# Optimization experiments

Hardware: AMD Instinct MI355X
Metric: run time of the kernel (lower is better)

## Reference

```python
import jax, jax.numpy as jnp
import numpy as np

DIM = 2048
CTX_DIM = 4096
NUM_HEADS = 16
HEAD_DIM = DIM // NUM_HEADS
EPS = 1e-6


def _rms_norm(x, weight, eps=EPS):
    # RMSNorm over last dim with learned weight (native dtype path for fp32)
    var = jnp.mean(jnp.square(x), axis=-1, keepdims=True)
    return x * jax.lax.rsqrt(var + eps) * weight


def setup_inputs() -> dict:
    key = jax.random.key(0)
    ks = jax.random.split(key, 12)
    B, L, S = 1, 8192, 512
    sd_q = 1.0 / np.sqrt(DIM)
    sd_c = 1.0 / np.sqrt(CTX_DIM)
    return {
        "x": jax.random.normal(ks[0], (B, L, DIM), dtype=jnp.float32),
        "context": jax.random.normal(ks[1], (B, S, CTX_DIM), dtype=jnp.float32),
        "Wq": jax.random.normal(ks[2], (DIM, DIM), dtype=jnp.float32) * sd_q,
        "bq": jax.random.normal(ks[3], (DIM,), dtype=jnp.float32) * 0.01,
        "Wk": jax.random.normal(ks[4], (CTX_DIM, DIM), dtype=jnp.float32) * sd_c,
        "bk": jax.random.normal(ks[5], (DIM,), dtype=jnp.float32) * 0.01,
        "Wv": jax.random.normal(ks[6], (CTX_DIM, DIM), dtype=jnp.float32) * sd_c,
        "bv": jax.random.normal(ks[7], (DIM,), dtype=jnp.float32) * 0.01,
        "Wo": jax.random.normal(ks[8], (DIM, DIM), dtype=jnp.float32) * sd_q,
        "bo": jax.random.normal(ks[9], (DIM,), dtype=jnp.float32) * 0.01,
        "g_q": jnp.ones((DIM,), dtype=jnp.float32),
        "g_k": jnp.ones((DIM,), dtype=jnp.float32),
    }


def reference(x, context, Wq, bq, Wk, bk, Wv, bv, Wo, bo, g_q, g_k):
    B, L, C = x.shape
    S = context.shape[1]
    # QKV projections + RMSNorm on Q,K (over full model dim, pre head split)
    q = _rms_norm(x @ Wq + bq, g_q)           # [B, L, C]
    k = _rms_norm(context @ Wk + bk, g_k)     # [B, S, C]
    v = context @ Wv + bv                     # [B, S, C]
    # split heads
    q = q.reshape(B, L, NUM_HEADS, HEAD_DIM)
    k = k.reshape(B, S, NUM_HEADS, HEAD_DIM)
    v = v.reshape(B, S, NUM_HEADS, HEAD_DIM)
    # non-causal SDPA
    scale = 1.0 / np.sqrt(HEAD_DIM)
    scores = jnp.einsum("blhd,bshd->bhls", q, k) * scale
    probs = jax.nn.softmax(scores, axis=-1)
    attn = jnp.einsum("bhls,bshd->blhd", probs, v).reshape(B, L, C)
    return attn @ Wo + bo
```

## Files before the change

kernel.cpp:

```cpp
#include <hip/hip_runtime.h>
#include <hip/hip_bf16.h>
#include <stdint.h>

#define L_SEQ 8192
#define S_SEQ 512
#define DIM   2048
#define CTX   4096
#define NH    16
#define HD    128

typedef __bf16 bf16_t;
typedef bf16_t bf16x8 __attribute__((ext_vector_type(8)));
typedef float  f32x4_t __attribute__((ext_vector_type(4)));
typedef float  f32x16_t __attribute__((ext_vector_type(16)));

__device__ __forceinline__ ushort f2b(float f) {
  union { float f; uint32_t u; } v; v.f = f;
  uint32_t u = v.u;
  uint32_t r = (u + 0x7fffu + ((u >> 16) & 1u)) >> 16;
  return (ushort)r;
}
__device__ __forceinline__ uint32_t pk2(float a, float b) {
  return (uint32_t)f2b(a) | ((uint32_t)f2b(b) << 16);
}
__device__ __forceinline__ float b2f(ushort u) {
  union { uint32_t u; float f; } v; v.u = ((uint32_t)u) << 16;
  return v.f;
}
__device__ __forceinline__ void gll16(const ushort* g, ushort* l) {
  __builtin_amdgcn_global_load_lds((const __attribute__((address_space(1))) void*)g,
                                   (__attribute__((address_space(3))) void*)l, 16, 0, 0);
}

__global__ __launch_bounds__(256) void k_cast(const float* __restrict__ in,
                                              ushort* __restrict__ out) {
  const size_t i = ((size_t)blockIdx.x * 256 + threadIdx.x) * 8;
  float4 a = *(const float4*)(in + i);
  float4 b = *(const float4*)(in + i + 4);
  uint4 r;
  r.x = pk2(a.x, a.y); r.y = pk2(a.z, a.w);
  r.z = pk2(b.x, b.y); r.w = pk2(b.z, b.w);
  *(uint4*)(out + i) = r;
}

__global__ __launch_bounds__(256) void k_tcast(const float* __restrict__ src,
                                               ushort* __restrict__ dst, int K, int N) {
  __shared__ float t[32][33];
  int tx = threadIdx.x, ty = threadIdx.y;
  int n0 = blockIdx.x * 32, k0 = blockIdx.y * 32;
#pragma unroll
  for (int i = 0; i < 4; i++)
    t[ty + 8 * i][tx] = src[(size_t)(k0 + ty + 8 * i) * N + n0 + tx];
  __syncthreads();
#pragma unroll
  for (int i = 0; i < 4; i++)
    dst[(size_t)(n0 + ty + 8 * i) * K + k0 + tx] = f2b(t[tx][ty + 8 * i]);
}

__global__ __launch_bounds__(256) void k_rmsnorm(const ushort* __restrict__ in,
                                                 ushort* __restrict__ out,
                                                 const float* __restrict__ g, float scale) {
  const int row = blockIdx.x, tid = threadIdx.x;
  uint4 v = *(const uint4*)(in + (size_t)row * DIM + tid * 8);
  const uint32_t* vu = (const uint32_t*)&v;
  float f[8];
#pragma unroll
  for (int i = 0; i < 4; i++) {
    f[2 * i]     = b2f((ushort)(vu[i] & 0xffffu));
    f[2 * i + 1] = b2f((ushort)(vu[i] >> 16));
  }
  float s = 0.f;
#pragma unroll
  for (int i = 0; i < 8; i++) s += f[i] * f[i];
#pragma unroll
  for (int off = 32; off; off >>= 1) s += __shfl_down(s, off);
  __shared__ float wsum[4];
  __shared__ float rtot;
  if ((tid & 63) == 0) wsum[tid >> 6] = s;
  __syncthreads();
  if (tid == 0)
    rtot = rsqrtf((wsum[0] + wsum[1] + wsum[2] + wsum[3]) * (1.0f / DIM) + 1e-6f);
  __syncthreads();
  const float rms = rtot * scale;
  const float* gp = g + tid * 8;
  float4 g0 = *(const float4*)gp, g1 = *(const float4*)(gp + 4);
  ushort r[8];
  r[0] = f2b(f[0] * rms * g0.x); r[1] = f2b(f[1] * rms * g0.y);
  r[2] = f2b(f[2] * rms * g0.z); r[3] = f2b(f[3] * rms * g0.w);
  r[4] = f2b(f[4] * rms * g1.x); r[5] = f2b(f[5] * rms * g1.y);
  r[6] = f2b(f[6] * rms * g1.z); r[7] = f2b(f[7] * rms * g1.w);
  *(uint4*)(out + (size_t)row * DIM + tid * 8) = *(uint4*)r;
}

template <int OUT_MODE>
__global__ __launch_bounds__(512, 2) void k_gemm256(const ushort* __restrict__ A,
                                                    const ushort* __restrict__ Bt,
                                                    const float* __restrict__ bias,
                                                    void* __restrict__ outp,
                                                    int M, int N, int K) {
  __shared__ __align__(16) ushort lds[65536];
  const int tid = threadIdx.x;
  const int l = tid & 63, wid = tid >> 6;
  const int wm = wid >> 2, wn = wid & 3;
  const int lr = l & 15, lq = l >> 4;

  const int nwg = gridDim.x * gridDim.y;
  const int bid = blockIdx.y * gridDim.x + blockIdx.x;
  const int swz = (bid & 7) * (nwg >> 3) + (bid >> 3);
  const int m0 = (swz / gridDim.x) * 256, n0 = (swz % gridDim.x) * 256;

  f32x4_t acc[8][4];
#pragma unroll
  for (int i = 0; i < 8; i++)
#pragma unroll
    for (int j = 0; j < 4; j++) acc[i][j] = f32x4_t{0.f, 0.f, 0.f, 0.f};

  const int srow = l >> 3;
  const int schunk = ((l & 7) ^ (srow & 7)) * 8;
  auto stage = [&](int buf, int tile, int mat, int h) {
    const ushort* gp = mat ? Bt : A;
    const int rn0 = mat ? n0 : m0;
    const size_t r0 = (size_t)(rn0 + h * 128 + wid * 8 + srow);
    const ushort* g0 = gp + r0 * K + tile * 64 + schunk;
    ushort* l0 = &lds[buf * 32768 + mat * 16384 + (h * 128 + wid * 8) * 64];
    gll16(g0, l0);
    gll16(g0 + (size_t)64 * K, l0 + 64 * 64);
  };

  auto rdA = [&](int buf, int mf, int ks) -> bf16x8 {
    const int R = wm * 128 + mf * 16 + lr;
    return *(const bf16x8*)(&lds[buf * 32768 + R * 64 + (((ks * 4 + lq) ^ (R & 7)) * 8)]);
  };
  auto rdB = [&](int buf, int nf, int ks) -> bf16x8 {
    const int R = wn * 64 + nf * 16 + lr;
    return *(const bf16x8*)(&lds[buf * 32768 + 16384 + R * 64 + (((ks * 4 + lq) ^ (R & 7)) * 8)]);
  };

  const int NT = K >> 6;
  stage(0, 0, 0, 0); stage(0, 0, 0, 1); stage(0, 0, 1, 0); stage(0, 0, 1, 1);

  bf16x8 a[4][2], a2[4][2], b[2][2], b2[2][2];
  for (int kt = 0; kt < NT; kt++) {
    const int cur = kt & 1, nxt = cur ^ 1;
    const bool pf = (kt + 1 < NT);
    if (pf) { stage(nxt, kt + 1, 0, 0); asm volatile("s_waitcnt vmcnt(2)" ::: "memory"); }
    else    { asm volatile("s_waitcnt vmcnt(0)" ::: "memory"); }
    __builtin_amdgcn_sched_barrier(0);
    __builtin_amdgcn_s_barrier();
    __builtin_amdgcn_sched_barrier(0);
#pragma unroll
    for (int mf = 0; mf < 4; mf++) { a[mf][0] = rdA(cur, mf, 0); a[mf][1] = rdA(cur, mf, 1); }
#pragma unroll
    for (int nf = 0; nf < 2; nf++) { b[nf][0] = rdB(cur, nf, 0); b[nf][1] = rdB(cur, nf, 1); }
    __builtin_amdgcn_s_setprio(1);
#pragma unroll
    for (int mf = 0; mf < 4; mf++)
#pragma unroll
      for (int nf = 0; nf < 2; nf++) {
        acc[mf][nf] = __builtin_amdgcn_mfma_f32_16x16x32_bf16(a[mf][0], b[nf][0], acc[mf][nf], 0, 0, 0);
        acc[mf][nf] = __builtin_amdgcn_mfma_f32_16x16x32_bf16(a[mf][1], b[nf][1], acc[mf][nf], 0, 0, 0);
      }
    __builtin_amdgcn_s_setprio(0);
    __builtin_amdgcn_sched_barrier(0);
    __builtin_amdgcn_s_barrier();
    __builtin_amdgcn_sched_barrier(0);
#pragma unroll
    for (int mf = 0; mf < 4; mf++) { a2[mf][0] = rdA(cur, mf + 4, 0); a2[mf][1] = rdA(cur, mf + 4, 1); }
    if (pf) stage(nxt, kt + 1, 0, 1);
    __builtin_amdgcn_sched_barrier(0);
    __builtin_amdgcn_s_barrier();
    __builtin_amdgcn_sched_barrier(0);
    __builtin_amdgcn_s_setprio(1);
#pragma unroll
    for (int mf = 0; mf < 4; mf++)
#pragma unroll
      for (int nf = 0; nf < 2; nf++) {
        acc[mf + 4][nf] = __builtin_amdgcn_mfma_f32_16x16x32_bf16(a2[mf][0], b[nf][0], acc[mf + 4][nf], 0, 0, 0);
        acc[mf + 4][nf] = __builtin_amdgcn_mfma_f32_16x16x32_bf16(a2[mf][1], b[nf][1], acc[mf + 4][nf], 0, 0, 0);
      }
    __builtin_amdgcn_s_setprio(0);
    __builtin_amdgcn_sched_barrier(0);
    __builtin_amdgcn_s_barrier();
    __builtin_amdgcn_sched_barrier(0);
#pragma unroll
    for (int nf = 0; nf < 2; nf++) { b2[nf][0] = rdB(cur, nf + 2, 0); b2[nf][1] = rdB(cur, nf + 2, 1); }
    if (pf) stage(nxt, kt + 1, 1, 0);
    __builtin_amdgcn_sched_barrier(0);
    __builtin_amdgcn_s_barrier();
    __builtin_amdgcn_sched_barrier(0);
    __builtin_amdgcn_s_setprio(1);
#pragma unroll
    for (int mf = 0; mf < 4; mf++)
#pragma unroll
      for (int nf = 0; nf < 2; nf++) {
        acc[mf + 4][nf + 2] = __builtin_amdgcn_mfma_f32_16x16x32_bf16(a2[mf][0], b2[nf][0], acc[mf + 4][nf + 2], 0, 0, 0);
        acc[mf + 4][nf + 2] = __builtin_amdgcn_mfma_f32_16x16x32_bf16(a2[mf][1], b2[nf][1], acc[mf + 4][nf + 2], 0, 0, 0);
      }
    __builtin_amdgcn_s_setprio(0);
    __builtin_amdgcn_sched_barrier(0);
    __builtin_amdgcn_s_barrier();
    __builtin_amdgcn_sched_barrier(0);
#pragma unroll
    for (int mf = 0; mf < 4; mf++) { a[mf][0] = rdA(cur, mf, 0); a[mf][1] = rdA(cur, mf, 1); }
    if (pf) stage(nxt, kt + 1, 1, 1);
    __builtin_amdgcn_sched_barrier(0);
    __builtin_amdgcn_s_barrier();
    __builtin_amdgcn_sched_barrier(0);
    __builtin_amdgcn_s_setprio(1);
#pragma unroll
    for (int mf = 0; mf < 4; mf++)
#pragma unroll
      for (int nf = 0; nf < 2; nf++) {
        acc[mf][nf + 2] = __builtin_amdgcn_mfma_f32_16x16x32_bf16(a[mf][0], b2[nf][0], acc[mf][nf + 2], 0, 0, 0);
        acc[mf][nf + 2] = __builtin_amdgcn_mfma_f32_16x16x32_bf16(a[mf][1], b2[nf][1], acc[mf][nf + 2], 0, 0, 0);
      }
    __builtin_amdgcn_s_setprio(0);
    __builtin_amdgcn_sched_barrier(0);
    __builtin_amdgcn_s_barrier();
    __builtin_amdgcn_sched_barrier(0);
  }

#pragma unroll
  for (int nf = 0; nf < 4; nf++) {
    const int col = n0 + wn * 64 + nf * 16 + lr;
    const float bv = bias[col];
#pragma unroll
    for (int mf = 0; mf < 8; mf++) {
#pragma unroll
      for (int r = 0; r < 4; r++) {
        const int row = m0 + wm * 128 + mf * 16 + lq * 4 + r;
        const float v = acc[mf][nf][r] + bv;
        if constexpr (OUT_MODE == 0)
          ((float*)outp)[(size_t)row * N + col] = v;
        else
          ((ushort*)outp)[(size_t)row * N + col] = f2b(v);
      }
    }
  }
}

template <int OUT_MODE>
__global__ __launch_bounds__(256) void k_gemm_bt(const ushort* __restrict__ A,
                                                 const ushort* __restrict__ Bt,
                                                 const float* __restrict__ bias,
                                                 const float* __restrict__ bias2,
                                                 void* __restrict__ outp,
                                                 void* __restrict__ outp2,
                                                 int M, int N, int K) {
  __shared__ __align__(16) ushort As[128 * 32];
  __shared__ __align__(16) ushort Bs[128 * 32];
  const int tid = threadIdx.x;
  const int l = tid & 63, wid = tid >> 6;
  const int wr = wid >> 1, wc = wid & 1;
  const int lr = l & 15, lq = l >> 4;

  const int nwg = gridDim.x * gridDim.y;
  const int bid = blockIdx.y * gridDim.x + blockIdx.x;
  const int swz = (bid & 7) * (nwg >> 3) + (bid >> 3);
  const int m0 = (swz / gridDim.x) * 128, n0 = (swz % gridDim.x) * 128;

  f32x4_t acc[4][4];
#pragma unroll
  for (int i = 0; i < 4; i++)
#pragma unroll
    for (int j = 0; j < 4; j++) acc[i][j] = f32x4_t{0.f, 0.f, 0.f, 0.f};

  const int srow = l >> 2;
  const int scol = (l & 3) * 8;
  const ushort* ga0 = A  + (size_t)(m0 + wid * 16 + srow) * K + scol;
  const ushort* ga1 = A  + (size_t)(m0 + (4 + wid) * 16 + srow) * K + scol;
  const ushort* gb0 = Bt + (size_t)(n0 + wid * 16 + srow) * K + scol;
  const ushort* gb1 = Bt + (size_t)(n0 + (4 + wid) * 16 + srow) * K + scol;
  ushort* la0 = &As[wid * 512];
  ushort* la1 = &As[(4 + wid) * 512];
  ushort* lb0 = &Bs[wid * 512];
  ushort* lb1 = &Bs[(4 + wid) * 512];

  const int NT = K >> 5;
  for (int kt = 0; kt < NT; kt++) {
    __syncthreads();
    const int ko = kt * 32;
    gll16(ga0 + ko, la0);
    gll16(ga1 + ko, la1);
    gll16(gb0 + ko, lb0);
    gll16(gb1 + ko, lb1);
    __syncthreads();

    bf16x8 af[4], bfr[4];
#pragma unroll
    for (int mi = 0; mi < 4; mi++)
      af[mi] = *(const bf16x8*)(&As[(wr * 64 + mi * 16 + lr) * 32 + lq * 8]);
#pragma unroll
    for (int ni = 0; ni < 4; ni++)
      bfr[ni] = *(const bf16x8*)(&Bs[(wc * 64 + ni * 16 + lr) * 32 + lq * 8]);
#pragma unroll
    for (int mi = 0; mi < 4; mi++)
#pragma unroll
      for (int ni = 0; ni < 4; ni++)
        acc[mi][ni] = __builtin_amdgcn_mfma_f32_16x16x32_bf16(af[mi], bfr[ni], acc[mi][ni], 0, 0, 0);
  }

#pragma unroll
  for (int mi = 0; mi < 4; mi++) {
#pragma unroll
    for (int ni = 0; ni < 4; ni++) {
      const int col = n0 + wc * 64 + ni * 16 + lr;
      float bv;
      if constexpr (OUT_MODE == 3) bv = (col < DIM) ? bias[col] : bias2[col - DIM];
      else bv = bias[col];
#pragma unroll
      for (int r = 0; r < 4; r++) {
        const int row = m0 + wr * 64 + mi * 16 + lq * 4 + r;
        const float v = acc[mi][ni][r] + bv;
        if constexpr (OUT_MODE == 0)
          ((float*)outp)[(size_t)row * N + col] = v;
        else if constexpr (OUT_MODE == 1)
          ((ushort*)outp)[(size_t)row * N + col] = f2b(v);
        else {
          if (col < DIM) ((ushort*)outp)[(size_t)row * DIM + col] = f2b(v);
          else ((ushort*)outp2)[(size_t)(col - DIM) * M + row] = f2b(v);
        }
      }
    }
  }
}

__global__ __launch_bounds__(256) void k_attn(const ushort* __restrict__ Qb,
                                              const ushort* __restrict__ Kb,
                                              const ushort* __restrict__ Vt,
                                              ushort* __restrict__ Ob) {
  __shared__ __align__(16) ushort smem[16384];
  ushort* Ks = smem;
  ushort* Vs = smem + 64 * 128;

  const int tid = threadIdx.x;
  const int l = tid & 63, wid = tid >> 6;
  const int lo = l & 31, hi = l >> 5;

  const int bid = blockIdx.x;
  const int swz = (bid & 7) * 128 + (bid >> 3);
  const int h = swz >> 6;
  const int q0 = (swz & 63) * 128 + wid * 32;

  bf16x8 qf[8];
  {
    const ushort* qp = Qb + (size_t)(q0 + lo) * DIM + h * HD + hi * 8;
#pragma unroll
    for (int ds = 0; ds < 8; ds++) qf[ds] = *(const bf16x8*)(qp + ds * 16);
  }

  f32x16_t o[4] = {};
  float m_run = -1e30f, l_run = 0.f;

  for (int kvb = 0; kvb < S_SEQ / 64; kvb++) {
    __syncthreads();
#pragma unroll
    for (int i = 0; i < 4; i++) {
      const int c = i * 256 + tid, row = c >> 4, cs = c & 15;
      gll16(Kb + (size_t)(kvb * 64 + row) * DIM + h * HD + ((cs ^ (row & 7)) * 8),
            Ks + c * 8);
    }
#pragma unroll
    for (int i = 0; i < 4; i++) {
      const int c = i * 256 + tid, row = c >> 3, cs = c & 7;
      gll16(Vt + (size_t)(h * HD + row) * S_SEQ + kvb * 64 + ((cs ^ (row & 7)) * 8),
            Vs + c * 8);
    }
    __syncthreads();

    f32x16_t sA = {}, sB = {};
#pragma unroll
    for (int ds = 0; ds < 8; ds++) {
      const int ch = ((hi + ds * 2) ^ (lo & 7)) * 8;
      bf16x8 kA = *(const bf16x8*)(Ks + lo * 128 + ch);
      bf16x8 kB = *(const bf16x8*)(Ks + (32 + lo) * 128 + ch);
      sA = __builtin_amdgcn_mfma_f32_32x32x16_bf16(kA, qf[ds], sA, 0, 0, 0);
      sB = __builtin_amdgcn_mfma_f32_32x32x16_bf16(kB, qf[ds], sB, 0, 0, 0);
    }

    float p[32];
#pragma unroll
    for (int i = 0; i < 16; i++) { p[i] = sA[i]; p[16 + i] = sB[i]; }
    float pm = p[0];
#pragma unroll
    for (int i = 1; i < 32; i++) pm = fmaxf(pm, p[i]);
    pm = fmaxf(pm, __shfl_xor(pm, 32));
    const float mn = fmaxf(m_run, pm);
    const float corr = __expf(m_run - mn);
    m_run = mn;
    float ps = 0.f;
#pragma unroll
    for (int i = 0; i < 32; i++) { p[i] = __expf(p[i] - mn); ps += p[i]; }
    ps += __shfl_xor(ps, 32);
    l_run = l_run * corr + ps;
#pragma unroll
    for (int nt = 0; nt < 4; nt++) o[nt] *= corr;

    uint32_t c[16];
#pragma unroll
    for (int j = 0; j < 16; j++) c[j] = pk2(p[2 * j], p[2 * j + 1]);
    bf16x8 pf[4];
#pragma unroll
    for (int s = 0; s < 4; s++) {
      const uint32_t ca = c[4 * s], cb = c[4 * s + 1], cc = c[4 * s + 2], cd = c[4 * s + 3];
      const uint32_t sa = __shfl_xor(ca, 32), sb = __shfl_xor(cb, 32);
      const uint32_t sc = __shfl_xor(cc, 32), sd = __shfl_xor(cd, 32);
      union { uint32_t u[4]; bf16x8 v; } f;
      f.u[0] = hi ? sc : ca; f.u[1] = hi ? sd : cb;
      f.u[2] = hi ? cc : sa; f.u[3] = hi ? cd : sb;
      pf[s] = f.v;
    }

#pragma unroll
    for (int nt = 0; nt < 4; nt++) {
      const int vrow = nt * 32 + lo;
#pragma unroll
      for (int s = 0; s < 4; s++) {
        bf16x8 vf = *(const bf16x8*)(Vs + vrow * 64 + (((s * 2 + hi) ^ (lo & 7)) * 8));
        o[nt] = __builtin_amdgcn_mfma_f32_32x32x16_bf16(vf, pf[s], o[nt], 0, 0, 0);
      }
    }
  }

  const float inv = 1.0f / l_run;
#pragma unroll
  for (int nt = 0; nt < 4; nt++) o[nt] *= inv;

  __syncthreads();
  float* tb = (float*)smem + wid * (32 * 33);
  const int q2 = l >> 1, dh = (l & 1) * 16;
#pragma unroll
  for (int nt = 0; nt < 4; nt++) {
#pragma unroll
    for (int r = 0; r < 16; r++)
      tb[lo * 33 + ((r & 3) + 8 * (r >> 2) + 4 * hi)] = o[nt][r];
    asm volatile("s_waitcnt lgkmcnt(0)" ::: "memory");
    __builtin_amdgcn_sched_barrier(0);
    ushort tmp[16];
#pragma unroll
    for (int j = 0; j < 16; j++) tmp[j] = f2b(tb[q2 * 33 + dh + j]);
    asm volatile("s_waitcnt lgkmcnt(0)" ::: "memory");
    __builtin_amdgcn_sched_barrier(0);
    const size_t oaddr = (size_t)(q0 + q2) * DIM + h * HD + nt * 32 + dh;
    *(uint4*)(Ob + oaddr) = *(uint4*)tmp;
    *(uint4*)(Ob + oaddr + 8) = *(uint4*)(tmp + 8);
  }
}

extern "C" void kernel_launch(void* const* d_in, const int* in_sizes, int n_in,
                              void* d_out, int out_size, void* d_ws, size_t ws_size,
                              hipStream_t stream) {
  const float* x   = (const float*)d_in[0];
  const float* ctx = (const float*)d_in[1];
  const float* Wq  = (const float*)d_in[2];
  const float* bq  = (const float*)d_in[3];
  const float* Wk  = (const float*)d_in[4];
  const float* bk  = (const float*)d_in[5];
  const float* Wv  = (const float*)d_in[6];
  const float* bv  = (const float*)d_in[7];
  const float* Wo  = (const float*)d_in[8];
  const float* bo  = (const float*)d_in[9];
  const float* gq  = (const float*)d_in[10];
  const float* gk  = (const float*)d_in[11];

  char* ws = (char*)d_ws;
  ushort* wqt   = (ushort*)(ws);
  ushort* wkt   = (ushort*)(ws + 8388608);
  ushort* wvt   = (ushort*)(ws + 25165824);
  ushort* wot   = (ushort*)(ws + 41943040);
  ushort* qb    = (ushort*)(ws + 50331648);
  ushort* kb    = (ushort*)(ws + 83886080);
  ushort* vt    = (ushort*)(ws + 85983232);
  ushort* xb    = (ushort*)(ws + 88080384);
  ushort* ctxb  = (ushort*)(ws + 88080384);
  ushort* qraw  = (ushort*)(ws + 121634816);
  ushort* kraw  = (ushort*)(ws + 121634816);
  ushort* attnb = (ushort*)(ws + 121634816);

  k_cast<<<L_SEQ * DIM / 8 / 256, 256, 0, stream>>>(x, xb);
  k_tcast<<<dim3(DIM / 32, DIM / 32), dim3(32, 8), 0, stream>>>(Wq, wqt, DIM, DIM);
  k_tcast<<<dim3(DIM / 32, CTX / 32), dim3(32, 8), 0, stream>>>(Wk, wkt, CTX, DIM);
  k_tcast<<<dim3(DIM / 32, CTX / 32), dim3(32, 8), 0, stream>>>(Wv, wvt, CTX, DIM);
  k_tcast<<<dim3(DIM / 32, DIM / 32), dim3(32, 8), 0, stream>>>(Wo, wot, DIM, DIM);

  k_gemm256<1><<<dim3(DIM / 256, L_SEQ / 256), 512, 0, stream>>>(xb, wqt, bq, qraw, L_SEQ, DIM, DIM);
  k_cast<<<S_SEQ * CTX / 8 / 256, 256, 0, stream>>>(ctx, ctxb);
  k_rmsnorm<<<L_SEQ, 256, 0, stream>>>(qraw, qb, gq, 0.08838834764831843f);
  k_gemm_bt<3><<<dim3(2 * DIM / 128, S_SEQ / 128), 256, 0, stream>>>(ctxb, wkt, bk, bv, kraw, vt, S_SEQ, 2 * DIM, CTX);
  k_rmsnorm<<<S_SEQ, 256, 0, stream>>>(kraw, kb, gk, 1.0f);
  k_attn<<<L_SEQ / 128 * NH, 256, 0, stream>>>(qb, kb, vt, attnb);
  k_gemm256<0><<<dim3(DIM / 256, L_SEQ / 256), 512, 0, stream>>>(attnb, wot, bo, d_out, L_SEQ, DIM, DIM);
}
```

Measured before the change: 363.8 us.

## Double-buffer LDS tiles in bt GEMM to overlap global loads with MFMA

Doubles the LDS A/B tile buffers in the transposed-B GEMM kernel and prefetches the next k-tile via direct global-to-LDS loads while the current tile is consumed. Explicit vmcnt waits and scheduling barriers replace the previous load-then-sync pattern, aiming to hide global memory latency behind MFMA work. This doubles LDS use per block, which may reduce occupancy, and it depends on the vmcnt(4) count matching the four outstanding loads.

```diff
diff --git a/kernel.cpp b/kernel.cpp
--- a/kernel.cpp
+++ b/kernel.cpp
@@ -247,8 +247,8 @@
                                                  void* __restrict__ outp,
                                                  void* __restrict__ outp2,
                                                  int M, int N, int K) {
-  __shared__ __align__(16) ushort As[128 * 32];
-  __shared__ __align__(16) ushort Bs[128 * 32];
+  __shared__ __align__(16) ushort As[2 * 128 * 32];
+  __shared__ __align__(16) ushort Bs[2 * 128 * 32];
   const int tid = threadIdx.x;
   const int l = tid & 63, wid = tid >> 6;
   const int wr = wid >> 1, wc = wid & 1;
@@ -271,33 +271,41 @@
   const ushort* ga1 = A  + (size_t)(m0 + (4 + wid) * 16 + srow) * K + scol;
   const ushort* gb0 = Bt + (size_t)(n0 + wid * 16 + srow) * K + scol;
   const ushort* gb1 = Bt + (size_t)(n0 + (4 + wid) * 16 + srow) * K + scol;
-  ushort* la0 = &As[wid * 512];
-  ushort* la1 = &As[(4 + wid) * 512];
-  ushort* lb0 = &Bs[wid * 512];
-  ushort* lb1 = &Bs[(4 + wid) * 512];
+
+  auto stageAB = [&](int buf, int kt) {
+    const int ko = kt * 32;
+    gll16(ga0 + ko, &As[buf * 4096 + wid * 512]);
+    gll16(ga1 + ko, &As[buf * 4096 + (4 + wid) * 512]);
+    gll16(gb0 + ko, &Bs[buf * 4096 + wid * 512]);
+    gll16(gb1 + ko, &Bs[buf * 4096 + (4 + wid) * 512]);
+  };
 
   const int NT = K >> 5;
+  stageAB(0, 0);
   for (int kt = 0; kt < NT; kt++) {
-    __syncthreads();
-    const int ko = kt * 32;
-    gll16(ga0 + ko, la0);
-    gll16(ga1 + ko, la1);
-    gll16(gb0 + ko, lb0);
-    gll16(gb1 + ko, lb1);
-    __syncthreads();
+    const int cur = kt & 1;
+    const bool pf = (kt + 1 < NT);
+    if (pf) { stageAB(cur ^ 1, kt + 1); asm volatile("s_waitcnt vmcnt(4)" ::: "memory"); }
+    else    { asm volatile("s_waitcnt vmcnt(0)" ::: "memory"); }
+    __builtin_amdgcn_sched_barrier(0);
+    __builtin_amdgcn_s_barrier();
+    __builtin_amdgcn_sched_barrier(0);
 
     bf16x8 af[4], bfr[4];
 #pragma unroll
     for (int mi = 0; mi < 4; mi++)
-      af[mi] = *(const bf16x8*)(&As[(wr * 64 + mi * 16 + lr) * 32 + lq * 8]);
+      af[mi] = *(const bf16x8*)(&As[cur * 4096 + (wr * 64 + mi * 16 + lr) * 32 + lq * 8]);
 #pragma unroll
     for (int ni = 0; ni < 4; ni++)
-      bfr[ni] = *(const bf16x8*)(&Bs[(wc * 64 + ni * 16 + lr) * 32 + lq * 8]);
+      bfr[ni] = *(const bf16x8*)(&Bs[cur * 4096 + (wc * 64 + ni * 16 + lr) * 32 + lq * 8]);
 #pragma unroll
     for (int mi = 0; mi < 4; mi++)
 #pragma unroll
       for (int ni = 0; ni < 4; ni++)
         acc[mi][ni] = __builtin_amdgcn_mfma_f32_16x16x32_bf16(af[mi], bfr[ni], acc[mi][ni], 0, 0, 0);
+    __builtin_amdgcn_sched_barrier(0);
+    __builtin_amdgcn_s_barrier();
+    __builtin_amdgcn_sched_barrier(0);
   }
 
 #pragma unroll
```

Result: faster. 355.5 us (-2.3%).
